# Optimization experiments

Measured on AMD Instinct MI355X. Metric: run time of the kernel, lower is better.

The kernel has to match this reference:

```python
import jax, jax.numpy as jnp
import numpy as np

EPS = 1e-5
NUM_HEADS = 16


def activation_quant(x):
    # 8-bit activation quant with straight-through estimator
    scale = 127.0 / jnp.clip(jnp.max(jnp.abs(x), axis=-1, keepdims=True), 1e-5, None)
    y = jnp.clip(jnp.round(x * scale), -128.0, 127.0) / scale
    return x + jax.lax.stop_gradient(y - x)


def weight_quant(w):
    # ternary {-1,0,1} weight quant with STE
    scale = 1.0 / jnp.clip(jnp.mean(jnp.abs(w)), 1e-5, None)
    wq = jnp.clip(jnp.round(w * scale), -1.0, 1.0) / scale
    return w + jax.lax.stop_gradient(wq - w)


def bitlinear(x, w):
    # F.layer_norm(x, x.shape[1:]): normalize over ALL dims except batch, no affine
    axes = tuple(range(1, x.ndim))
    mu = jnp.mean(x, axis=axes, keepdims=True)
    var = jnp.var(x, axis=axes, keepdims=True)
    xn = (x - mu) * jax.lax.rsqrt(var + EPS)
    return jnp.einsum('bnd,od->bno', activation_quant(xn), weight_quant(w))


def layer_norm(x, gamma, beta):
    mu = jnp.mean(x, axis=-1, keepdims=True)
    var = jnp.var(x, axis=-1, keepdims=True)
    return (x - mu) * jax.lax.rsqrt(var + EPS) * gamma + beta


def setup_inputs() -> dict:
    key = jax.random.key(0)
    k0, k1, k2 = jax.random.split(key, 3)
    B, N, D = 2, 2048, 1024
    return {
        't': jnp.zeros((1,), jnp.float32),
        'x': jax.random.normal(k0, (B, N, D), jnp.float32),
        'w_qkv': jax.random.normal(k1, (3 * D, D), jnp.float32) * 0.02,
        'w_out': jax.random.normal(k2, (D, D), jnp.float32) * 0.02,
        'gamma': jnp.ones((D,), jnp.float32),
        'beta': jnp.zeros((D,), jnp.float32),
    }


def reference(t, x, w_qkv, w_out, gamma, beta):
    B, N, D = x.shape
    H = NUM_HEADS
    hd = D // H
    scale = hd ** -0.5
    h = layer_norm(x, gamma, beta)                     # [B,N,D]
    qkv = bitlinear(h, w_qkv).reshape(B, N, 3, H, hd)   # [B,N,3,H,hd]
    qkv = jnp.transpose(qkv, (2, 0, 3, 1, 4))           # [3,B,H,N,hd]
    q, k, v = qkv[0], qkv[1], qkv[2]
    attn = jax.nn.softmax(jnp.einsum('bhnd,bhmd->bhnm', q, k) * scale, axis=-1)
    out = jnp.einsum('bhnm,bhmd->bhnd', attn, v)        # [B,H,N,hd]
    out = jnp.transpose(out, (0, 2, 1, 3)).reshape(B, N, D)
    return bitlinear(out, w_out)
```

## Files before the change

kernel.cpp:

```cpp
#include <hip/hip_runtime.h>
#include <hip/hip_bf16.h>
#include <hip/hip_fp16.h>
#include <math.h>

typedef __hip_bfloat16 bf16;
typedef int   i32x4 __attribute__((ext_vector_type(4)));
typedef float f32x4 __attribute__((ext_vector_type(4)));
typedef short bfx8  __attribute__((ext_vector_type(8)));

#define EPSV 1e-5f
#define NROWS 4096
#define DIM   1024
#define NSEQ  2048

__device__ __forceinline__ float ldv(const void* p, size_t i, int dt){
  if (dt == 0) return ((const float*)p)[i];
  if (dt == 1) return __bfloat162float(((const bf16*)p)[i]);
  return __half2float(((const __half*)p)[i]);
}

__device__ __forceinline__ float blk_sum(float v, float* sm){
  #pragma unroll
  for (int o = 32; o > 0; o >>= 1) v += __shfl_xor(v, o, 64);
  __syncthreads();
  if ((threadIdx.x & 63) == 0) sm[threadIdx.x >> 6] = v;
  __syncthreads();
  return sm[0] + sm[1] + sm[2] + sm[3];
}
__device__ __forceinline__ double blk_sum_d(double v, double* sm){
  #pragma unroll
  for (int o = 32; o > 0; o >>= 1) v += __shfl_xor(v, o, 64);
  __syncthreads();
  if ((threadIdx.x & 63) == 0) sm[threadIdx.x >> 6] = v;
  __syncthreads();
  return sm[0] + sm[1] + sm[2] + sm[3];
}
__device__ __forceinline__ float blk_max(float v, float* sm){
  #pragma unroll
  for (int o = 32; o > 0; o >>= 1) v = fmaxf(v, __shfl_xor(v, o, 64));
  __syncthreads();
  if ((threadIdx.x & 63) == 0) sm[threadIdx.x >> 6] = v;
  __syncthreads();
  return fmaxf(fmaxf(sm[0], sm[1]), fmaxf(sm[2], sm[3]));
}

__global__ void setup_gb(const void* c0, const void* c1, int* flags,
                         float* gamma_f, float* beta_f){
  __shared__ int sdt, sgf;
  if (threadIdx.x == 0){
    unsigned u0 = *(const unsigned*)c0;
    int gfirst = (u0 != 0u) ? 1 : 0;
    const unsigned short* g = (const unsigned short*)(gfirst ? c0 : c1);
    int dt;
    if (g[0] == 0x3F80) dt = 1;
    else if (g[0] == 0x3C00) dt = 2;
    else dt = 0;
    flags[0] = dt; flags[1] = gfirst;
    sdt = dt; sgf = gfirst;
  }
  __syncthreads();
  int dt = sdt;
  const void* g = sgf ? c0 : c1;
  const void* b = sgf ? c1 : c0;
  for (int i = threadIdx.x; i < DIM; i += blockDim.x){
    gamma_f[i] = ldv(g, i, dt);
    beta_f[i]  = ldv(b, i, dt);
  }
}

__global__ __launch_bounds__(256) void ln_rows(const void* __restrict__ x,
                                               const float* __restrict__ gamma_f,
                                               const float* __restrict__ beta_f,
                                               float* __restrict__ h,
                                               double* __restrict__ lnp,
                                               const int* __restrict__ flags){
  __shared__ float sm[4];
  __shared__ double smd[4];
  int dt = flags[0];
  int row = blockIdx.x;
  int tid = threadIdx.x;
  float v[4]; float s = 0.f;
  if (dt == 0){
    float4 v4 = ((const float4*)x)[(size_t)row*256 + tid];
    v[0]=v4.x; v[1]=v4.y; v[2]=v4.z; v[3]=v4.w;
  } else {
    size_t base = (size_t)row * DIM;
    #pragma unroll
    for (int i = 0; i < 4; ++i) v[i] = ldv(x, base + 4*tid + i, dt);
  }
  #pragma unroll
  for (int i = 0; i < 4; ++i) s += v[i];
  s = blk_sum(s, sm);
  float mu = s * (1.f/1024.f);
  float d2 = 0.f;
  #pragma unroll
  for (int i = 0; i < 4; ++i){ float d = v[i] - mu; d2 += d*d; }
  d2 = blk_sum(d2, sm);
  float rs = rsqrtf(d2 * (1.f/1024.f) + EPSV);
  float4 gm = ((const float4*)gamma_f)[tid];
  float4 bt = ((const float4*)beta_f)[tid];
  float hv[4];
  hv[0] = (v[0]-mu)*rs*gm.x + bt.x;
  hv[1] = (v[1]-mu)*rs*gm.y + bt.y;
  hv[2] = (v[2]-mu)*rs*gm.z + bt.z;
  hv[3] = (v[3]-mu)*rs*gm.w + bt.w;
  ((float4*)h)[(size_t)row*256 + tid] = make_float4(hv[0],hv[1],hv[2],hv[3]);
  double hs = 0.0, hq = 0.0;
  #pragma unroll
  for (int i = 0; i < 4; ++i){ hs += (double)hv[i]; hq += (double)hv[i]*(double)hv[i]; }
  hs = blk_sum_d(hs, smd);
  hq = blk_sum_d(hq, smd);
  if (tid == 0){ lnp[2*row] = hs; lnp[2*row + 1] = hq; }
}

__global__ __launch_bounds__(256) void abs_reduce(const void* __restrict__ w, int n,
                                                  double* __restrict__ part,
                                                  const int* __restrict__ flags){
  __shared__ double smd[4];
  int dt = flags[0];
  double s = 0.0;
  if (dt == 0){
    const float4* w4 = (const float4*)w;
    int n4 = n >> 2;
    for (int i = blockIdx.x*256 + threadIdx.x; i < n4; i += gridDim.x*256){
      float4 v = w4[i];
      s += (double)(fabsf(v.x) + fabsf(v.y)) + (double)(fabsf(v.z) + fabsf(v.w));
    }
  } else {
    for (int i = blockIdx.x*256 + threadIdx.x; i < n; i += gridDim.x*256)
      s += (double)fabsf(ldv(w, i, dt));
  }
  s = blk_sum_d(s, smd);
  if (threadIdx.x == 0) part[blockIdx.x] = s;
}

__global__ __launch_bounds__(256) void finalize1(float* acc,
                                                 const double* __restrict__ lnp,
                                                 const double* __restrict__ awp1,
                                                 const double* __restrict__ awp2){
  __shared__ double smd[4];
  int tid = threadIdx.x;
  double s0=0, q0=0, s1=0, q1=0, a1=0, a2=0;
  for (int i = tid; i < 2048; i += 256){
    s0 += lnp[2*i];          q0 += lnp[2*i + 1];
    s1 += lnp[2*(i+2048)];   q1 += lnp[2*(i+2048) + 1];
  }
  for (int i = tid; i < 512; i += 256){ a1 += awp1[i]; a2 += awp2[i]; }
  s0 = blk_sum_d(s0, smd);  q0 = blk_sum_d(q0, smd);
  s1 = blk_sum_d(s1, smd);  q1 = blk_sum_d(q1, smd);
  a1 = blk_sum_d(a1, smd);  a2 = blk_sum_d(a2, smd);
  if (tid == 0){
    const double cnt = 2097152.0;
    double mu0 = s0/cnt, var0 = q0/cnt - mu0*mu0;
    double mu1 = s1/cnt, var1 = q1/cnt - mu1*mu1;
    acc[16] = (float)mu0; acc[17] = (float)(1.0 / sqrt(var0 + 1e-5));
    acc[18] = (float)mu1; acc[19] = (float)(1.0 / sqrt(var1 + 1e-5));
    acc[20] = (float)(1.0 / fmax(a1 / (3.0*1024.0*1024.0), 1e-5));
    acc[21] = (float)(1.0 / fmax(a2 / (1024.0*1024.0), 1e-5));
  }
}

__global__ __launch_bounds__(256) void finalize2(float* acc,
                                                 const double* __restrict__ atp){
  __shared__ double smd[4];
  int tid = threadIdx.x;
  double s0=0, q0=0, s1=0, q1=0;
  for (int i = tid; i < 512; i += 256){
    s0 += atp[2*i];          q0 += atp[2*i + 1];
    s1 += atp[2*(i+512)];    q1 += atp[2*(i+512) + 1];
  }
  s0 = blk_sum_d(s0, smd);  q0 = blk_sum_d(q0, smd);
  s1 = blk_sum_d(s1, smd);  q1 = blk_sum_d(q1, smd);
  if (tid == 0){
    const double cnt = 2097152.0;
    double mu0 = s0/cnt, var0 = q0/cnt - mu0*mu0;
    double mu1 = s1/cnt, var1 = q1/cnt - mu1*mu1;
    acc[22] = (float)mu0; acc[23] = (float)(1.0 / sqrt(var0 + 1e-5));
    acc[24] = (float)mu1; acc[25] = (float)(1.0 / sqrt(var1 + 1e-5));
  }
}

__global__ __launch_bounds__(256) void act_quant_i8(const float* __restrict__ buf,
                                                    signed char* __restrict__ qout,
                                                    float* __restrict__ rscale,
                                                    const float* __restrict__ acc,
                                                    int statOff){
  __shared__ float sm[4];
  int row = blockIdx.x;
  int b = row >> 11;
  float mu = acc[statOff + 2*b], rs = acc[statOff + 2*b + 1];
  int tid = threadIdx.x;
  float4 v4 = ((const float4*)buf)[(size_t)row*256 + tid];
  float v[4] = {(v4.x-mu)*rs, (v4.y-mu)*rs, (v4.z-mu)*rs, (v4.w-mu)*rs};
  float am = fmaxf(fmaxf(fabsf(v[0]), fabsf(v[1])), fmaxf(fabsf(v[2]), fabsf(v[3])));
  am = blk_max(am, sm);
  am = fmaxf(am, 1e-5f);
  float s127 = 127.f / am;
  unsigned pk = 0;
  #pragma unroll
  for (int i = 0; i < 4; ++i){
    float q = rintf(v[i] * s127);
    q = fminf(fmaxf(q, -128.f), 127.f);
    pk |= ((unsigned)(unsigned char)(signed char)q) << (8*i);
  }
  ((unsigned*)qout)[(size_t)row*256 + tid] = pk;
  if (tid == 0) rscale[row] = am * (1.f/127.f);
}

__global__ __launch_bounds__(256) void w_quant_i8(const void* __restrict__ w,
                                                  signed char* __restrict__ wq, int n,
                                                  const float* __restrict__ acc, int sidx,
                                                  const int* __restrict__ flags){
  int dt = flags[0];
  float scale = acc[sidx];
  if (dt == 0){
    const float4* w4 = (const float4*)w;
    int n4 = n >> 2;
    for (int i = blockIdx.x*256 + threadIdx.x; i < n4; i += gridDim.x*256){
      float4 v = w4[i];
      float vv[4] = {v.x, v.y, v.z, v.w};
      unsigned pk = 0;
      #pragma unroll
      for (int j = 0; j < 4; ++j){
        float q = rintf(vv[j] * scale);
        q = fminf(fmaxf(q, -1.f), 1.f);
        pk |= ((unsigned)(unsigned char)(signed char)q) << (8*j);
      }
      ((unsigned*)wq)[i] = pk;
    }
  } else {
    for (int i = blockIdx.x*256 + threadIdx.x; i < n; i += gridDim.x*256){
      float q = rintf(ldv(w, i, dt) * scale);
      q = fminf(fmaxf(q, -1.f), 1.f);
      wq[i] = (signed char)q;
    }
  }
}

__global__ __launch_bounds__(256) void gemm_i8(const signed char* __restrict__ A,
                                               const signed char* __restrict__ W,
                                               const float* __restrict__ rscale,
                                               const float* __restrict__ acc, int sidx,
                                               float* __restrict__ Cf,
                                               bf16* __restrict__ Cb,
                                               int ldc, int writeBf, float q_prescale){
  __shared__ __attribute__((aligned(16))) signed char Asl[128][80];
  __shared__ __attribute__((aligned(16))) signed char Bsl[128][80];
  int tid = threadIdx.x, lane = tid & 63, w = tid >> 6;
  int wr = w >> 1, wc = w & 1;

  int nwgx = gridDim.x;
  int flat = blockIdx.y * nwgx + blockIdx.x;
  int nwg  = nwgx * gridDim.y;
  int cpx  = nwg >> 3;
  int swz  = (flat & 7) * cpx + (flat >> 3);
  int r0 = (swz / nwgx) * 128, o0 = (swz % nwgx) * 128;

  i32x4 zz = {0,0,0,0};
  i32x4 accv[4][4];
  #pragma unroll
  for (int m = 0; m < 4; ++m)
    #pragma unroll
    for (int n = 0; n < 4; ++n) accv[m][n] = zz;

  int sr0 = tid >> 2, sr1 = sr0 + 64;
  int sc  = (tid & 3) * 16;

  i32x4 a0, a1, b0, b1;
  a0 = *(const i32x4*)(A + (size_t)(r0 + sr0)*1024 + sc);
  a1 = *(const i32x4*)(A + (size_t)(r0 + sr1)*1024 + sc);
  b0 = *(const i32x4*)(W + (size_t)(o0 + sr0)*1024 + sc);
  b1 = *(const i32x4*)(W + (size_t)(o0 + sr1)*1024 + sc);

  for (int k0 = 0; k0 < 1024; k0 += 64){
    __syncthreads();
    *(i32x4*)&Asl[sr0][sc] = a0;
    *(i32x4*)&Asl[sr1][sc] = a1;
    *(i32x4*)&Bsl[sr0][sc] = b0;
    *(i32x4*)&Bsl[sr1][sc] = b1;
    __syncthreads();
    if (k0 + 64 < 1024){
      int kn = k0 + 64;
      a0 = *(const i32x4*)(A + (size_t)(r0 + sr0)*1024 + kn + sc);
      a1 = *(const i32x4*)(A + (size_t)(r0 + sr1)*1024 + kn + sc);
      b0 = *(const i32x4*)(W + (size_t)(o0 + sr0)*1024 + kn + sc);
      b1 = *(const i32x4*)(W + (size_t)(o0 + sr1)*1024 + kn + sc);
    }
    i32x4 af[4], bfr[4];
    #pragma unroll
    for (int m = 0; m < 4; ++m)
      af[m] = *(const i32x4*)&Asl[wr*64 + m*16 + (lane & 15)][(lane >> 4) * 16];
    #pragma unroll
    for (int n = 0; n < 4; ++n)
      bfr[n] = *(const i32x4*)&Bsl[wc*64 + n*16 + (lane & 15)][(lane >> 4) * 16];
    #pragma unroll
    for (int m = 0; m < 4; ++m)
      #pragma unroll
      for (int n = 0; n < 4; ++n)
        accv[m][n] = __builtin_amdgcn_mfma_i32_16x16x64_i8(af[m], bfr[n], accv[m][n], 0, 0, 0);
  }

  float wsc = acc[sidx];
  float cs = (o0 < 1024) ? q_prescale : 1.0f;
  float rf[4][4];
  #pragma unroll
  for (int m = 0; m < 4; ++m)
    #pragma unroll
    for (int r = 0; r < 4; ++r)
      rf[m][r] = rscale[r0 + wr*64 + m*16 + ((lane >> 4) << 2) + r] / wsc * cs;

  #pragma unroll
  for (int m = 0; m < 4; ++m)
    #pragma unroll
    for (int n = 0; n < 4; ++n)
      #pragma unroll
      for (int r = 0; r < 4; ++r){
        float val = (float)accv[m][n][r] * rf[m][r];
        size_t row = (size_t)(r0 + wr*64 + m*16 + ((lane >> 4) << 2) + r);
        int col = o0 + wc*64 + n*16 + (lane & 15);
        if (writeBf) Cb[row * ldc + col] = __float2bfloat16(val);
        else         Cf[row * ldc + col] = val;
      }
}

__global__ __launch_bounds__(256) void attn_mfma(const bf16* __restrict__ qkv,
                                                 float* __restrict__ out,
                                                 double* __restrict__ atp){
  __shared__ __attribute__((aligned(16))) unsigned short K_lds[64][72];
  __shared__ __attribute__((aligned(16))) unsigned short Vt_lds[64][72];
  __shared__ __attribute__((aligned(16))) unsigned short P_lds[4][16][72];
  __shared__ double smd[4];

  int tid = threadIdx.x, lane = tid & 63, w = tid >> 6;
  int l15 = lane & 15, g = lane >> 4;

  int flat = blockIdx.y * 32 + blockIdx.x;
  int slot = flat & 7, idx = flat >> 3;
  int bh = slot * 4 + (idx >> 5);
  int qx = idx & 31;
  int b = bh >> 4, h = bh & 15;
  int n0 = qx * 64;
  const unsigned short* qg = (const unsigned short*)qkv;

  bfx8 qf[2];
  #pragma unroll
  for (int s = 0; s < 2; ++s){
    int qrow = b*NSEQ + n0 + w*16 + l15;
    qf[s] = *(const bfx8*)(qg + (size_t)qrow*3072 + h*64 + g*8 + s*32);
  }

  float m_run = -INFINITY, l_run = 0.f;
  f32x4 zf = {0.f, 0.f, 0.f, 0.f};
  f32x4 acco[4];
  #pragma unroll
  for (int n = 0; n < 4; ++n) acco[n] = zf;

  int krow = lane;
  int r2 = tid & 31, dwin = tid >> 5;

  bfx8 kc0, kc1, vv0, vv1;
  auto LOADT = [&](int kt){
    size_t kvb = (size_t)(b*NSEQ + kt*64);
    kc0 = *(const bfx8*)(qg + (kvb + krow)*3072 + 1024 + h*64 + w*8);
    kc1 = *(const bfx8*)(qg + (kvb + krow)*3072 + 1024 + h*64 + (w + 4)*8);
    vv0 = *(const bfx8*)(qg + (kvb + 2*r2    )*3072 + 2048 + h*64 + dwin*8);
    vv1 = *(const bfx8*)(qg + (kvb + 2*r2 + 1)*3072 + 2048 + h*64 + dwin*8);
  };
  LOADT(0);

  for (int kt = 0; kt < NSEQ/64; ++kt){
    __syncthreads();
    *(bfx8*)&K_lds[krow][w*8]      = kc0;
    *(bfx8*)&K_lds[krow][w*8 + 32] = kc1;
    #pragma unroll
    for (int u = 0; u < 8; ++u){
      unsigned word = (unsigned)(unsigned short)vv0[u] |
                      ((unsigned)(unsigned short)vv1[u] << 16);
      *(unsigned*)&Vt_lds[dwin*8 + u][2*r2] = word;
    }
    __syncthreads();
    if (kt + 1 < NSEQ/64) LOADT(kt + 1);

    f32x4 sacc[4];
    #pragma unroll
    for (int f = 0; f < 4; ++f) sacc[f] = zf;
    #pragma unroll
    for (int f = 0; f < 4; ++f)
      #pragma unroll
      for (int s = 0; s < 2; ++s){
        bfx8 kb = *(const bfx8*)&K_lds[f*16 + l15][g*8 + s*32];
        sacc[f] = __builtin_amdgcn_mfma_f32_16x16x32_bf16(kb, qf[s], sacc[f], 0, 0, 0);
      }

    float pm = sacc[0][0];
    #pragma unroll
    for (int f = 0; f < 4; ++f)
      #pragma unroll
      for (int r = 0; r < 4; ++r) pm = fmaxf(pm, sacc[f][r]);
    pm = fmaxf(pm, __shfl_xor(pm, 16, 64));
    pm = fmaxf(pm, __shfl_xor(pm, 32, 64));
    if (__any(pm > m_run + 8.f)){
      float mnew = fmaxf(m_run, pm);
      float corr = __expf(m_run - mnew);
      m_run = mnew;
      l_run *= corr;
      float ca[4];
      #pragma unroll
      for (int r = 0; r < 4; ++r) ca[r] = __shfl(corr, 4*g + r, 64);
      #pragma unroll
      for (int n = 0; n < 4; ++n)
        #pragma unroll
        for (int r = 0; r < 4; ++r) acco[n][r] *= ca[r];
    }
    float p[4][4]; float ts = 0.f;
    #pragma unroll
    for (int f = 0; f < 4; ++f)
      #pragma unroll
      for (int r = 0; r < 4; ++r){
        p[f][r] = __expf(sacc[f][r] - m_run);
        ts += p[f][r];
      }
    ts += __shfl_xor(ts, 16, 64);
    ts += __shfl_xor(ts, 32, 64);
    l_run += ts;

    #pragma unroll
    for (int f = 0; f < 4; ++f)
      #pragma unroll
      for (int rp = 0; rp < 2; ++rp){
        bf16 pb0 = __float2bfloat16(p[f][2*rp]);
        bf16 pb1 = __float2bfloat16(p[f][2*rp+1]);
        unsigned pk = (unsigned)*reinterpret_cast<unsigned short*>(&pb0) |
                      ((unsigned)*reinterpret_cast<unsigned short*>(&pb1) << 16);
        *(unsigned*)&P_lds[w][l15][16*f + 4*g + 2*rp] = pk;
      }

    bfx8 pa[2];
    #pragma unroll
    for (int s = 0; s < 2; ++s)
      pa[s] = *(const bfx8*)&P_lds[w][l15][g*8 + s*32];
    #pragma unroll
    for (int n = 0; n < 4; ++n)
      #pragma unroll
      for (int s = 0; s < 2; ++s){
        bfx8 vb = *(const bfx8*)&Vt_lds[n*16 + l15][g*8 + s*32];
        acco[n] = __builtin_amdgcn_mfma_f32_16x16x32_bf16(pa[s], vb, acco[n], 0, 0, 0);
      }
  }

  float il = 1.f / l_run;
  float ila[4];
  #pragma unroll
  for (int r = 0; r < 4; ++r) ila[r] = __shfl(il, 4*g + r, 64);
  double ssum = 0.0, ssq = 0.0;
  #pragma unroll
  for (int n = 0; n < 4; ++n)
    #pragma unroll
    for (int r = 0; r < 4; ++r){
      float o = acco[n][r] * ila[r];
      int orow = b*NSEQ + n0 + w*16 + 4*g + r;
      out[(size_t)orow * DIM + h*64 + n*16 + l15] = o;
      ssum += (double)o; ssq += (double)o * (double)o;
    }
  ssum = blk_sum_d(ssum, smd);
  ssq  = blk_sum_d(ssq, smd);
  if (tid == 0){
    int bflat = bh * 32 + qx;
    atp[2*bflat] = ssum; atp[2*bflat + 1] = ssq;
  }
}

extern "C" void kernel_launch(void* const* d_in, const int* in_sizes, int n_in,
                              void* d_out, int out_size, void* d_ws, size_t ws_size,
                              hipStream_t stream) {
  int ix = -1, iwq = -1, iwo = -1, ig0 = -1, ig1 = -1;
  for (int i = 0; i < n_in; ++i){
    int s = in_sizes[i];
    if      (s == 4194304) ix  = i;
    else if (s == 3145728) iwq = i;
    else if (s == 1048576) iwo = i;
    else if (s == 1024){ if (ig0 < 0) ig0 = i; else ig1 = i; }
  }
  if (ix < 0 || iwq < 0 || iwo < 0 || ig0 < 0 || ig1 < 0){ ix=1; iwq=2; iwo=3; ig0=4; ig1=5; }
  const void* x     = d_in[ix];
  const void* w_qkv = d_in[iwq];
  const void* w_out = d_in[iwo];
  const void* g0    = d_in[ig0];
  const void* g1    = d_in[ig1];

  char* ws = (char*)d_ws;
  float*  acc     = (float*)ws;
  int*    flags   = (int*)(ws + 448);
  float*  gamma_f = (float*)(ws + 4096);
  float*  beta_f  = (float*)(ws + 8192);
  float*  rscale1 = (float*)(ws + 12288);
  float*  rscale2 = (float*)(ws + 28672);
  double* lnp     = (double*)(ws + 65536);
  double* awp1    = (double*)(ws + 131072);
  double* awp2    = (double*)(ws + 135168);
  double* atp     = (double*)(ws + 139264);
  float*        h      = (float*)      (ws + (1u<<20));
  signed char*  h_i8   = (signed char*)(ws + (17u<<20));
  signed char*  wqk_i8 = (signed char*)(ws + (21u<<20));
  signed char*  wqo_i8 = (signed char*)(ws + (24u<<20));
  bf16*         qkvb   = (bf16*)       (ws + (25u<<20));
  signed char*  a2_i8  = (signed char*)(ws + (49u<<20));
  float*        aout   = h;

  setup_gb<<<1, 256, 0, stream>>>(g0, g1, flags, gamma_f, beta_f);
  ln_rows<<<NROWS, 256, 0, stream>>>(x, gamma_f, beta_f, h, lnp, flags);
  abs_reduce<<<512, 256, 0, stream>>>(w_qkv, 3*DIM*DIM, awp1, flags);
  abs_reduce<<<512, 256, 0, stream>>>(w_out, DIM*DIM, awp2, flags);
  finalize1<<<1, 256, 0, stream>>>(acc, lnp, awp1, awp2);
  act_quant_i8<<<NROWS, 256, 0, stream>>>(h, h_i8, rscale1, acc, 16);
  w_quant_i8<<<512, 256, 0, stream>>>(w_qkv, wqk_i8, 3*DIM*DIM, acc, 20, flags);
  w_quant_i8<<<512, 256, 0, stream>>>(w_out, wqo_i8, DIM*DIM, acc, 21, flags);
  gemm_i8<<<dim3(24, 32), 256, 0, stream>>>(h_i8, wqk_i8, rscale1, acc, 20,
                                            nullptr, qkvb, 3072, 1, 0.125f);
  attn_mfma<<<dim3(32, 32), 256, 0, stream>>>(qkvb, aout, atp);
  finalize2<<<1, 256, 0, stream>>>(acc, atp);
  act_quant_i8<<<NROWS, 256, 0, stream>>>(aout, a2_i8, rscale2, acc, 22);
  gemm_i8<<<dim3(8, 32), 256, 0, stream>>>(a2_i8, wqo_i8, rscale2, acc, 21,
                                           (float*)d_out, nullptr, 1024, 0, 1.0f);
}
```

Before: 169.2 us.

## XOR-swizzle attention LDS tiles and raise wave priority around MFMA blocks

Replaces the padded (72-column) K, transposed V and P LDS tiles in the attention kernel with unpadded 64-column tiles addressed through an XOR swizzle on 16-byte chunks. The aim is to avoid bank conflicts without wasting LDS. It also wraps the MFMA groups in both the int8 GEMM and the attention kernel with s_setprio, so waves issuing matrix ops get scheduling priority. The swizzle has to match exactly between writers and readers, and any mismatch produces wrong results.

Result: faster. 164.9 us (-2.5%).

```diff
diff --git a/kernel.cpp b/kernel.cpp
--- a/kernel.cpp
+++ b/kernel.cpp
@@ -293,11 +293,13 @@
     #pragma unroll
     for (int n = 0; n < 4; ++n)
       bfr[n] = *(const i32x4*)&Bsl[wc*64 + n*16 + (lane & 15)][(lane >> 4) * 16];
+    __builtin_amdgcn_s_setprio(1);
     #pragma unroll
     for (int m = 0; m < 4; ++m)
       #pragma unroll
       for (int n = 0; n < 4; ++n)
         accv[m][n] = __builtin_amdgcn_mfma_i32_16x16x64_i8(af[m], bfr[n], accv[m][n], 0, 0, 0);
+    __builtin_amdgcn_s_setprio(0);
   }
 
   float wsc = acc[sidx];
@@ -326,13 +328,14 @@
 __global__ __launch_bounds__(256) void attn_mfma(const bf16* __restrict__ qkv,
                                                  float* __restrict__ out,
                                                  double* __restrict__ atp){
-  __shared__ __attribute__((aligned(16))) unsigned short K_lds[64][72];
-  __shared__ __attribute__((aligned(16))) unsigned short Vt_lds[64][72];
-  __shared__ __attribute__((aligned(16))) unsigned short P_lds[4][16][72];
+  __shared__ __attribute__((aligned(16))) unsigned short K_lds[64][64];
+  __shared__ __attribute__((aligned(16))) unsigned short Vt_lds[64][64];
+  __shared__ __attribute__((aligned(16))) unsigned short P_lds[4][16][64];
   __shared__ double smd[4];
 
   int tid = threadIdx.x, lane = tid & 63, w = tid >> 6;
   int l15 = lane & 15, g = lane >> 4;
+  int h7 = l15 & 7;
 
   int flat = blockIdx.y * 32 + blockIdx.x;
   int slot = flat & 7, idx = flat >> 3;
@@ -341,6 +344,10 @@
   int b = bh >> 4, h = bh & 15;
   int n0 = qx * 64;
   const unsigned short* qg = (const unsigned short*)qkv;
+
+  char* kB = (char*)K_lds;
+  char* vB = (char*)Vt_lds;
+  char* pB = (char*)P_lds + w*2048;
 
   bfx8 qf[2];
   #pragma unroll
@@ -370,13 +377,16 @@
 
   for (int kt = 0; kt < NSEQ/64; ++kt){
     __syncthreads();
-    *(bfx8*)&K_lds[krow][w*8]      = kc0;
-    *(bfx8*)&K_lds[krow][w*8 + 32] = kc1;
+    {
+      int lh7 = lane & 7;
+      *(bfx8*)(kB + lane*128 + (((w    ) ^ lh7) << 4)) = kc0;
+      *(bfx8*)(kB + lane*128 + (((w + 4) ^ lh7) << 4)) = kc1;
+    }
     #pragma unroll
     for (int u = 0; u < 8; ++u){
       unsigned word = (unsigned)(unsigned short)vv0[u] |
                       ((unsigned)(unsigned short)vv1[u] << 16);
-      *(unsigned*)&Vt_lds[dwin*8 + u][2*r2] = word;
+      *(unsigned*)(vB + (dwin*8 + u)*128 + ((4*r2) ^ (u << 4))) = word;
     }
     __syncthreads();
     if (kt + 1 < NSEQ/64) LOADT(kt + 1);
@@ -385,12 +395,14 @@
     #pragma unroll
     for (int f = 0; f < 4; ++f) sacc[f] = zf;
     #pragma unroll
-    for (int f = 0; f < 4; ++f)
-      #pragma unroll
-      for (int s = 0; s < 2; ++s){
-        bfx8 kb = *(const bfx8*)&K_lds[f*16 + l15][g*8 + s*32];
-        sacc[f] = __builtin_amdgcn_mfma_f32_16x16x32_bf16(kb, qf[s], sacc[f], 0, 0, 0);
-      }
+    for (int f = 0; f < 4; ++f){
+      bfx8 kb0 = *(const bfx8*)(kB + (f*16 + l15)*128 + (((g    ) ^ h7) << 4));
+      bfx8 kb1 = *(const bfx8*)(kB + (f*16 + l15)*128 + (((g + 4) ^ h7) << 4));
+      __builtin_amdgcn_s_setprio(1);
+      sacc[f] = __builtin_amdgcn_mfma_f32_16x16x32_bf16(kb0, qf[0], sacc[f], 0, 0, 0);
+      sacc[f] = __builtin_amdgcn_mfma_f32_16x16x32_bf16(kb1, qf[1], sacc[f], 0, 0, 0);
+      __builtin_amdgcn_s_setprio(0);
+    }
 
     float pm = sacc[0][0];
     #pragma unroll
@@ -432,20 +444,22 @@
         bf16 pb1 = __float2bfloat16(p[f][2*rp+1]);
         unsigned pk = (unsigned)*reinterpret_cast<unsigned short*>(&pb0) |
                       ((unsigned)*reinterpret_cast<unsigned short*>(&pb1) << 16);
-        *(unsigned*)&P_lds[w][l15][16*f + 4*g + 2*rp] = pk;
+        *(unsigned*)(pB + l15*128 + ((32*f + 8*g + 4*rp) ^ (h7 << 4))) = pk;
       }
 
     bfx8 pa[2];
     #pragma unroll
     for (int s = 0; s < 2; ++s)
-      pa[s] = *(const bfx8*)&P_lds[w][l15][g*8 + s*32];
-    #pragma unroll
-    for (int n = 0; n < 4; ++n)
-      #pragma unroll
-      for (int s = 0; s < 2; ++s){
-        bfx8 vb = *(const bfx8*)&Vt_lds[n*16 + l15][g*8 + s*32];
-        acco[n] = __builtin_amdgcn_mfma_f32_16x16x32_bf16(pa[s], vb, acco[n], 0, 0, 0);
-      }
+      pa[s] = *(const bfx8*)(pB + l15*128 + (((g + 4*s) ^ h7) << 4));
+    #pragma unroll
+    for (int n = 0; n < 4; ++n){
+      bfx8 vb0 = *(const bfx8*)(vB + (n*16 + l15)*128 + (((g    ) ^ h7) << 4));
+      bfx8 vb1 = *(const bfx8*)(vB + (n*16 + l15)*128 + (((g + 4) ^ h7) << 4));
+      __builtin_amdgcn_s_setprio(1);
+      acco[n] = __builtin_amdgcn_mfma_f32_16x16x32_bf16(pa[0], vb0, acco[n], 0, 0, 0);
+      acco[n] = __builtin_amdgcn_mfma_f32_16x16x32_bf16(pa[1], vb1, acco[n], 0, 0, 0);
+      __builtin_amdgcn_s_setprio(0);
+    }
   }
 
   float il = 1.f / l_run;
```
